# Optimization experiments

Hardware: AMD Instinct MI355X
Metric: run time of the kernel (lower is better)

The kernel has to match this reference:

```python
import jax, jax.numpy as jnp
import numpy as np

B, T, D, NH = 2, 2048, 2048, 16
HID = D  # hidden_dim must equal emb_dim for the source's fc2(x1) to type-check
HD = D // NH
EPS = 1e-5


def setup_inputs() -> dict:
    key = jax.random.key(0)
    ks = jax.random.split(key, 16)
    s = 0.02
    inp = {
        "x": jax.random.normal(ks[0], (B, T, D), jnp.float32),
        "Wq": jax.random.normal(ks[1], (D, D), jnp.float32) * s,
        "bq": jnp.zeros((D,), jnp.float32),
        "Wk": jax.random.normal(ks[2], (D, D), jnp.float32) * s,
        "bk": jnp.zeros((D,), jnp.float32),
        "Wv": jax.random.normal(ks[3], (D, D), jnp.float32) * s,
        "bv": jnp.zeros((D,), jnp.float32),
        "Wo": jax.random.normal(ks[4], (D, D), jnp.float32) * s,
        "bo": jnp.zeros((D,), jnp.float32),
        "scale1": jnp.ones((D,), jnp.float32),
        "scale2": jnp.ones((D,), jnp.float32),
        "W1": jax.random.normal(ks[5], (D, HID), jnp.float32) * s,
        "W2": jax.random.normal(ks[6], (D, HID), jnp.float32) * s,  # fc2: Linear(emb_dim, hidden_dim)
        "W3": jax.random.normal(ks[7], (HID, D), jnp.float32) * s,
    }
    return inp


def _rmsnorm(x, scale):
    m = jnp.mean(x * x, axis=-1, keepdims=True)
    return scale * (x * jax.lax.rsqrt(m + EPS))


def _attention(x, Wq, bq, Wk, bk, Wv, bv, Wo, bo):
    b, t, _ = x.shape
    q = (x @ Wq + bq).reshape(b, t, NH, HD)
    k = (x @ Wk + bk).reshape(b, t, NH, HD)
    v = (x @ Wv + bv).reshape(b, t, NH, HD)
    # energy: [B, H, T, T]; softmax over keys, scaled by 1/sqrt(head_dim); NO causal mask in source
    energy = jnp.einsum("bqhd,bkhd->bhqk", q, k) / jnp.sqrt(jnp.float32(HD))
    attn = jax.nn.softmax(energy, axis=-1)
    out = jnp.einsum("bhqk,bkhd->bqhd", attn, v).reshape(b, t, D)
    return out @ Wo + bo


def _ffn(x, W1, W2, W3):
    x1 = x @ W1                       # [B,T,HID]
    x2 = x1 @ W2                      # source quirk: fc2 applied to x1 (hidden_dim == emb_dim)
    return (x1 * jax.nn.sigmoid(x1) * x2) @ W3


def reference(x, Wq, bq, Wk, bk, Wv, bv, Wo, bo, scale1, scale2, W1, W2, W3):
    shortcut = x
    h = _rmsnorm(x, scale1)
    h = _attention(h, Wq, bq, Wk, bk, Wv, bv, Wo, bo)
    h = shortcut + h
    h = _rmsnorm(h, scale2)
    h = _ffn(h, W1, W2, W3)
    # source adds the ORIGINAL input again (shortcut never reassigned)
    return h + shortcut
```

## Files before the change

kernel.cpp:

```cpp
#include <hip/hip_runtime.h>

typedef __bf16 bf16x8 __attribute__((ext_vector_type(8)));
typedef __bf16 bf16x4v __attribute__((ext_vector_type(4)));
typedef float  f32x4  __attribute__((ext_vector_type(4)));

#define LDS_AS(p) ((__attribute__((address_space(3))) void*)(p))
#define GLB_AS(p) ((const __attribute__((address_space(1))) void*)(p))

struct TP { const float* s[7]; __bf16* d[7]; };
__global__ __launch_bounds__(256) void transpose_convert_all(TP p) {
  const float* __restrict__ W = p.s[blockIdx.z];
  __bf16* __restrict__ Wt = p.d[blockIdx.z];
  __shared__ float tile[32][33];
  const int tx = threadIdx.x & 31, ty = threadIdx.x >> 5;
  const int n0 = blockIdx.x * 32, k0 = blockIdx.y * 32;
#pragma unroll
  for (int j = 0; j < 4; ++j)
    tile[ty + j * 8][tx] = W[(size_t)(k0 + ty + j * 8) * 2048 + n0 + tx];
  __syncthreads();
#pragma unroll
  for (int j = 0; j < 4; ++j)
    Wt[(size_t)(n0 + ty + j * 8) * 2048 + k0 + tx] = (__bf16)tile[tx][ty + j * 8];
}

__global__ __launch_bounds__(256) void rmsnorm_k(
    const float* __restrict__ x, const float* __restrict__ scale,
    __bf16* __restrict__ out) {
  const int row = blockIdx.x, t = threadIdx.x;
  const float4* xr = (const float4*)(x + (size_t)row * 2048);
  float4 a = xr[t], b2 = xr[t + 256];
  float ss = a.x * a.x + a.y * a.y + a.z * a.z + a.w * a.w +
             b2.x * b2.x + b2.y * b2.y + b2.z * b2.z + b2.w * b2.w;
#pragma unroll
  for (int ofs = 32; ofs; ofs >>= 1) ss += __shfl_xor(ss, ofs, 64);
  __shared__ float red[4];
  if ((t & 63) == 0) red[t >> 6] = ss;
  __syncthreads();
  ss = red[0] + red[1] + red[2] + red[3];
  const float rs = rsqrtf(ss * (1.f / 2048.f) + 1e-5f);
  const float4* sr = (const float4*)scale;
  float4 s1 = sr[t], s2 = sr[t + 256];
  __bf16* orow = out + (size_t)row * 2048;
  orow[t * 4 + 0] = (__bf16)(a.x * rs * s1.x);
  orow[t * 4 + 1] = (__bf16)(a.y * rs * s1.y);
  orow[t * 4 + 2] = (__bf16)(a.z * rs * s1.z);
  orow[t * 4 + 3] = (__bf16)(a.w * rs * s1.w);
  orow[(t + 256) * 4 + 0] = (__bf16)(b2.x * rs * s2.x);
  orow[(t + 256) * 4 + 1] = (__bf16)(b2.y * rs * s2.y);
  orow[(t + 256) * 4 + 2] = (__bf16)(b2.z * rs * s2.z);
  orow[(t + 256) * 4 + 3] = (__bf16)(b2.w * rs * s2.w);
}

template <bool OUTF32, bool HASBIAS, bool HASRES, bool SILU>
__global__ __launch_bounds__(256) void gemm_bt(
    const __bf16* __restrict__ A, const __bf16* __restrict__ Bt,
    const float* __restrict__ bias, const float* __restrict__ res,
    const __bf16* __restrict__ ew, void* __restrict__ Cout,
    int M, int N, int Kd) {
  __shared__ __attribute__((aligned(16))) __bf16 As[2][128 * 32];
  __shared__ __attribute__((aligned(16))) __bf16 Bs[2][128 * 32];
  const int tid = threadIdx.x;
  const int w = tid >> 6, l = tid & 63;
  const int M0 = blockIdx.y * 128, N0 = blockIdx.x * 128;
  const int wr = w >> 1, wc = w & 1;
  const int lm = l & 15, lq = l >> 4;

  f32x4 acc[4][4];
#pragma unroll
  for (int mt = 0; mt < 4; ++mt)
#pragma unroll
    for (int nt = 0; nt < 4; ++nt)
#pragma unroll
      for (int e = 0; e < 4; ++e) acc[mt][nt][e] = 0.f;

  const int offA0 = (w * 2 + 0) * 1024 + l * 16;
  const int offA1 = (w * 2 + 1) * 1024 + l * 16;
  const int row0 = offA0 >> 6, kb0 = offA0 & 63;
  const int row1 = offA1 >> 6, kb1 = offA1 & 63;
  const int nIt = Kd >> 5;

  auto stage = [&](int k0, int bsel) {
    const char* ga0 = (const char*)(A + (size_t)(M0 + row0) * Kd + k0) + kb0;
    const char* ga1 = (const char*)(A + (size_t)(M0 + row1) * Kd + k0) + kb1;
    const char* gb0 = (const char*)(Bt + (size_t)(N0 + row0) * Kd + k0) + kb0;
    const char* gb1 = (const char*)(Bt + (size_t)(N0 + row1) * Kd + k0) + kb1;
    __builtin_amdgcn_global_load_lds(GLB_AS(ga0), LDS_AS(((char*)As[bsel]) + (w * 2 + 0) * 1024), 16, 0, 0);
    __builtin_amdgcn_global_load_lds(GLB_AS(ga1), LDS_AS(((char*)As[bsel]) + (w * 2 + 1) * 1024), 16, 0, 0);
    __builtin_amdgcn_global_load_lds(GLB_AS(gb0), LDS_AS(((char*)Bs[bsel]) + (w * 2 + 0) * 1024), 16, 0, 0);
    __builtin_amdgcn_global_load_lds(GLB_AS(gb1), LDS_AS(((char*)Bs[bsel]) + (w * 2 + 1) * 1024), 16, 0, 0);
  };

  stage(0, 0);
  for (int it = 0; it < nIt; ++it) {
    __syncthreads();
    if (it + 1 < nIt) stage((it + 1) * 32, (it + 1) & 1);
    const __bf16* Ab = As[it & 1];
    const __bf16* Bb = Bs[it & 1];
    bf16x8 af[4], bfr[4];
#pragma unroll
    for (int mt = 0; mt < 4; ++mt)
      af[mt] = *(const bf16x8*)(Ab + (wr * 64 + mt * 16 + lm) * 32 + lq * 8);
#pragma unroll
    for (int nt = 0; nt < 4; ++nt)
      bfr[nt] = *(const bf16x8*)(Bb + (wc * 64 + nt * 16 + lm) * 32 + lq * 8);
#pragma unroll
    for (int mt = 0; mt < 4; ++mt)
#pragma unroll
      for (int nt = 0; nt < 4; ++nt)
        acc[mt][nt] = __builtin_amdgcn_mfma_f32_16x16x32_bf16(af[mt], bfr[nt], acc[mt][nt], 0, 0, 0);
  }

  const int lr = lq * 4;
#pragma unroll
  for (int mt = 0; mt < 4; ++mt) {
#pragma unroll
    for (int nt = 0; nt < 4; ++nt) {
      const int col = N0 + wc * 64 + nt * 16 + lm;
      float bv = 0.f;
      if (HASBIAS) bv = bias[col];
#pragma unroll
      for (int i = 0; i < 4; ++i) {
        const int row = M0 + wr * 64 + mt * 16 + lr + i;
        const size_t off = (size_t)row * N + col;
        float v = acc[mt][nt][i] + bv;
        if (HASRES) v += res[off];
        if (SILU) {
          const float x1v = (float)ew[off];
          v = x1v * (1.f / (1.f + __expf(-x1v))) * v;
        }
        if (OUTF32) ((float*)Cout)[off] = v;
        else ((__bf16*)Cout)[off] = (__bf16)v;
      }
    }
  }
}

__global__ __launch_bounds__(256) void gemm_qkv(
    const __bf16* __restrict__ A, const __bf16* __restrict__ Bt,
    const float* __restrict__ bq, const float* __restrict__ bk,
    const float* __restrict__ bv,
    __bf16* __restrict__ Qout, __bf16* __restrict__ Kout,
    __bf16* __restrict__ Vtout, int Kd) {
  __shared__ __attribute__((aligned(16))) __bf16 As[2][128 * 32];
  __shared__ __attribute__((aligned(16))) __bf16 Bs[2][128 * 32];
  const int tid = threadIdx.x;
  const int w = tid >> 6, l = tid & 63;
  const int M0 = blockIdx.y * 128, N0 = blockIdx.x * 128;
  const int wr = w >> 1, wc = w & 1;
  const int lm = l & 15, lq = l >> 4;

  f32x4 acc[4][4];
#pragma unroll
  for (int mt = 0; mt < 4; ++mt)
#pragma unroll
    for (int nt = 0; nt < 4; ++nt)
#pragma unroll
      for (int e = 0; e < 4; ++e) acc[mt][nt][e] = 0.f;

  const int offA0 = (w * 2 + 0) * 1024 + l * 16;
  const int offA1 = (w * 2 + 1) * 1024 + l * 16;
  const int row0 = offA0 >> 6, kb0 = offA0 & 63;
  const int row1 = offA1 >> 6, kb1 = offA1 & 63;
  const int nIt = Kd >> 5;

  auto stage = [&](int k0, int bsel) {
    const char* ga0 = (const char*)(A + (size_t)(M0 + row0) * Kd + k0) + kb0;
    const char* ga1 = (const char*)(A + (size_t)(M0 + row1) * Kd + k0) + kb1;
    const char* gb0 = (const char*)(Bt + (size_t)(N0 + row0) * Kd + k0) + kb0;
    const char* gb1 = (const char*)(Bt + (size_t)(N0 + row1) * Kd + k0) + kb1;
    __builtin_amdgcn_global_load_lds(GLB_AS(ga0), LDS_AS(((char*)As[bsel]) + (w * 2 + 0) * 1024), 16, 0, 0);
    __builtin_amdgcn_global_load_lds(GLB_AS(ga1), LDS_AS(((char*)As[bsel]) + (w * 2 + 1) * 1024), 16, 0, 0);
    __builtin_amdgcn_global_load_lds(GLB_AS(gb0), LDS_AS(((char*)Bs[bsel]) + (w * 2 + 0) * 1024), 16, 0, 0);
    __builtin_amdgcn_global_load_lds(GLB_AS(gb1), LDS_AS(((char*)Bs[bsel]) + (w * 2 + 1) * 1024), 16, 0, 0);
  };

  stage(0, 0);
  for (int it = 0; it < nIt; ++it) {
    __syncthreads();
    if (it + 1 < nIt) stage((it + 1) * 32, (it + 1) & 1);
    const __bf16* Ab = As[it & 1];
    const __bf16* Bb = Bs[it & 1];
    bf16x8 af[4], bfr[4];
#pragma unroll
    for (int mt = 0; mt < 4; ++mt)
      af[mt] = *(const bf16x8*)(Ab + (wr * 64 + mt * 16 + lm) * 32 + lq * 8);
#pragma unroll
    for (int nt = 0; nt < 4; ++nt)
      bfr[nt] = *(const bf16x8*)(Bb + (wc * 64 + nt * 16 + lm) * 32 + lq * 8);
#pragma unroll
    for (int mt = 0; mt < 4; ++mt)
#pragma unroll
      for (int nt = 0; nt < 4; ++nt)
        acc[mt][nt] = __builtin_amdgcn_mfma_f32_16x16x32_bf16(af[mt], bfr[nt], acc[mt][nt], 0, 0, 0);
  }

  const int lr = lq * 4;
  const int seg = N0 >> 11;
  const int nbase = N0 & 2047;
  const float* bb = (seg == 0) ? bq : ((seg == 1) ? bk : bv);
  if (seg < 2) {
    __bf16* dst = (seg == 0) ? Qout : Kout;
#pragma unroll
    for (int mt = 0; mt < 4; ++mt) {
#pragma unroll
      for (int nt = 0; nt < 4; ++nt) {
        const int col = nbase + wc * 64 + nt * 16 + lm;
        const float bvv = bb[col];
#pragma unroll
        for (int i = 0; i < 4; ++i) {
          const int row = M0 + wr * 64 + mt * 16 + lr + i;
          dst[(size_t)row * 2048 + col] = (__bf16)(acc[mt][nt][i] + bvv);
        }
      }
    }
  } else {
#pragma unroll
    for (int mt = 0; mt < 4; ++mt) {
#pragma unroll
      for (int nt = 0; nt < 4; ++nt) {
        const int col = nbase + wc * 64 + nt * 16 + lm;
        const float bvv = bb[col];
        const int rw0 = M0 + wr * 64 + mt * 16 + lr;
        const int bidx = rw0 >> 11, tok = rw0 & 2047;
        bf16x4v pk;
#pragma unroll
        for (int i = 0; i < 4; ++i) pk[i] = (__bf16)(acc[mt][nt][i] + bvv);
        *(bf16x4v*)(Vtout + ((size_t)(bidx * 2048 + col)) * 2048 + tok) = pk;
      }
    }
  }
}

__global__ __launch_bounds__(256, 2) void attn_mfma(
    const __bf16* __restrict__ Q, const __bf16* __restrict__ K,
    const __bf16* __restrict__ Vt, __bf16* __restrict__ O) {
  __shared__ __attribute__((aligned(16))) char KsL[2][16 * 1024];
  __shared__ __attribute__((aligned(16))) char VsL[2][16 * 1024];

  const int t = threadIdx.x;
  const int w = t >> 6, l = t & 63;
  const int lm = l & 15, quad = l >> 4;
  const int h = blockIdx.y, b = blockIdx.z;
  const int q0 = blockIdx.x * 128;
  const size_t Ds = 2048;
  const size_t hoff = (size_t)h * 128;
  const size_t bbase = (size_t)b * 2048;
  const int sl16 = ((lm << 2) | quad) * 16;
  const float SCL = 0.08838834764831845f * 1.4426950408889634f;

  const int krow = l >> 2, kcol = (l & 3) * 8;
  const int vth = l & 3, vd = l >> 2;

  bf16x8 qf[2][4];
#pragma unroll
  for (int ntq = 0; ntq < 2; ++ntq)
#pragma unroll
    for (int ks = 0; ks < 4; ++ks)
      qf[ntq][ks] = *(const bf16x8*)(Q + (bbase + q0 + w * 32 + ntq * 16 + lm) * Ds + hoff + ks * 32 + quad * 8);

  f32x4 oacc[2][8];
#pragma unroll
  for (int ntq = 0; ntq < 2; ++ntq)
#pragma unroll
    for (int nv = 0; nv < 8; ++nv)
#pragma unroll
      for (int e = 0; e < 4; ++e) oacc[ntq][nv][e] = 0.f;
  float lpart[2] = {0.f, 0.f};

  bf16x8 vreg[4];

  auto loadV = [&](int kt) {
#pragma unroll
    for (int i = 0; i < 4; ++i) {
      const int chunk = w * 4 + i;
      const int nv = chunk >> 1, c = chunk & 1;
      vreg[i] = *(const bf16x8*)(Vt + (bbase + hoff + nv * 16 + vd) * Ds + kt + c * 32 + vth * 8);
    }
  };
  auto stageK = [&](int kt, char* Kb) {
#pragma unroll
    for (int i = 0; i < 4; ++i) {
      const __bf16* src = K + (bbase + kt + i * 16 + krow) * Ds + hoff + w * 32 + kcol;
      __builtin_amdgcn_global_load_lds(GLB_AS(src), LDS_AS(Kb + (i * 4 + w) * 1024), 16, 0, 0);
    }
  };
  auto writeV = [&](char* Vb) {
    const int s0off = ((vd << 2) | ((vth & 1) * 2)) * 16 + (vth >> 1) * 8;
#pragma unroll
    for (int i = 0; i < 4; ++i) {
      char* base = Vb + (w * 4 + i) * 1024;
      uint4 u = *(const uint4*)&vreg[i];
      *(uint2*)(base + s0off) = make_uint2(u.x, u.y);
      *(uint2*)(base + s0off + 16) = make_uint2(u.z, u.w);
    }
  };

  loadV(0);
  stageK(0, KsL[0]);
  writeV(VsL[0]);

  for (int it = 0; it < 32; ++it) {
    __syncthreads();
    const int cur = it & 1;
    const bool more = (it + 1) < 32;
    if (more) { loadV((it + 1) * 64); stageK((it + 1) * 64, KsL[(it + 1) & 1]); }

    const char* Kb = KsL[cur];
    const char* Vb = VsL[cur];

    f32x4 st[4][2];
#pragma unroll
    for (int mtk = 0; mtk < 4; ++mtk)
#pragma unroll
      for (int ntq = 0; ntq < 2; ++ntq)
#pragma unroll
        for (int e = 0; e < 4; ++e) st[mtk][ntq][e] = 0.f;
#pragma unroll
    for (int ks = 0; ks < 4; ++ks) {
#pragma unroll
      for (int mtk = 0; mtk < 4; ++mtk) {
        bf16x8 kf = *(const bf16x8*)(Kb + (mtk * 4 + ks) * 1024 + sl16);
        st[mtk][0] = __builtin_amdgcn_mfma_f32_16x16x32_bf16(kf, qf[0][ks], st[mtk][0], 0, 0, 0);
        st[mtk][1] = __builtin_amdgcn_mfma_f32_16x16x32_bf16(kf, qf[1][ks], st[mtk][1], 0, 0, 0);
      }
    }

#pragma unroll
    for (int c = 0; c < 2; ++c) {
      bf16x8 pf[2];
#pragma unroll
      for (int ntq = 0; ntq < 2; ++ntq) {
#pragma unroll
        for (int half = 0; half < 2; ++half) {
          const f32x4 sv = st[c * 2 + half][ntq];
#pragma unroll
          for (int r = 0; r < 4; ++r) {
            const float p = exp2f(sv[r] * SCL);
            const __bf16 pb = (__bf16)p;
            pf[ntq][half * 4 + r] = pb;
            lpart[ntq] += (float)pb;
          }
        }
      }
#pragma unroll
      for (int nv = 0; nv < 8; ++nv) {
        bf16x8 vf = *(const bf16x8*)(Vb + (nv * 2 + c) * 1024 + sl16);
        oacc[0][nv] = __builtin_amdgcn_mfma_f32_16x16x32_bf16(pf[0], vf, oacc[0][nv], 0, 0, 0);
        oacc[1][nv] = __builtin_amdgcn_mfma_f32_16x16x32_bf16(pf[1], vf, oacc[1][nv], 0, 0, 0);
      }
    }

    if (more) writeV(VsL[(it + 1) & 1]);
  }

  float linv[2];
#pragma unroll
  for (int ntq = 0; ntq < 2; ++ntq) {
    float v = lpart[ntq];
    v += __shfl_xor(v, 16, 64);
    v += __shfl_xor(v, 32, 64);
    linv[ntq] = 1.f / v;
  }
  float oinv[2][4];
#pragma unroll
  for (int ntq = 0; ntq < 2; ++ntq)
#pragma unroll
    for (int r = 0; r < 4; ++r)
      oinv[ntq][r] = __shfl(linv[ntq], quad * 4 + r, 64);

#pragma unroll
  for (int ntq = 0; ntq < 2; ++ntq)
#pragma unroll
    for (int nv = 0; nv < 8; ++nv)
#pragma unroll
      for (int r = 0; r < 4; ++r) {
        const int qrow = q0 + w * 32 + ntq * 16 + quad * 4 + r;
        O[(bbase + qrow) * Ds + hoff + nv * 16 + lm] = (__bf16)(oacc[ntq][nv][r] * oinv[ntq][r]);
      }
}

extern "C" void kernel_launch(void* const* d_in, const int* in_sizes, int n_in,
                              void* d_out, int out_size, void* d_ws, size_t ws_size,
                              hipStream_t stream) {
  const float* x      = (const float*)d_in[0];
  const float* Wq     = (const float*)d_in[1];
  const float* bq     = (const float*)d_in[2];
  const float* Wk     = (const float*)d_in[3];
  const float* bk     = (const float*)d_in[4];
  const float* Wv     = (const float*)d_in[5];
  const float* bv     = (const float*)d_in[6];
  const float* Wo     = (const float*)d_in[7];
  const float* bo     = (const float*)d_in[8];
  const float* scale1 = (const float*)d_in[9];
  const float* scale2 = (const float*)d_in[10];
  const float* W1     = (const float*)d_in[11];
  const float* W2     = (const float*)d_in[12];
  const float* W3     = (const float*)d_in[13];

  const int M = 4096, N = 2048, Kd = 2048;
  char* ws = (char*)d_ws;
  const size_t WT_B = (size_t)2048 * 2048 * 2;
  const size_t ACT_B = (size_t)4096 * 2048 * 2;
  __bf16* wt[7];
  size_t off = 0;
  for (int i = 0; i < 7; ++i) { wt[i] = (__bf16*)(ws + off); off += WT_B; }
  __bf16* hn1  = (__bf16*)(ws + off); off += ACT_B;
  __bf16* Qb   = (__bf16*)(ws + off); off += ACT_B;
  __bf16* Kb   = (__bf16*)(ws + off); off += ACT_B;
  __bf16* VtG  = (__bf16*)(ws + off); off += ACT_B;
  __bf16* attn = (__bf16*)(ws + off); off += ACT_B;
  __bf16* hn2  = (__bf16*)(ws + off); off += ACT_B;
  __bf16* x1b  = (__bf16*)(ws + off); off += ACT_B;
  __bf16* fmb  = (__bf16*)(ws + off); off += ACT_B;

  dim3 tb(256);
  {
    TP p;
    p.s[0] = Wq; p.s[1] = Wk; p.s[2] = Wv; p.s[3] = Wo; p.s[4] = W1; p.s[5] = W2; p.s[6] = W3;
    for (int i = 0; i < 7; ++i) p.d[i] = wt[i];
    transpose_convert_all<<<dim3(64, 64, 7), tb, 0, stream>>>(p);
  }

  rmsnorm_k<<<4096, tb, 0, stream>>>(x, scale1, hn1);

  gemm_qkv<<<dim3(6144 / 128, M / 128), tb, 0, stream>>>(
      hn1, wt[0], bq, bk, bv, Qb, Kb, VtG, Kd);

  dim3 ag(2048 / 128, 16, 2);
  attn_mfma<<<ag, tb, 0, stream>>>(Qb, Kb, VtG, attn);

  dim3 gg(N / 128, M / 128);
  gemm_bt<true, true, true, false><<<gg, tb, 0, stream>>>(attn, wt[3], bo, x, nullptr, d_out, M, N, Kd);

  rmsnorm_k<<<4096, tb, 0, stream>>>((const float*)d_out, scale2, hn2);

  gemm_bt<false, false, false, false><<<gg, tb, 0, stream>>>(hn2, wt[4], nullptr, nullptr, nullptr, x1b, M, N, Kd);
  gemm_bt<false, false, false, true><<<gg, tb, 0, stream>>>(x1b, wt[5], nullptr, nullptr, x1b, fmb, M, N, Kd);
  gemm_bt<true, false, true, false><<<gg, tb, 0, stream>>>(fmb, wt[6], nullptr, x, nullptr, d_out, M, N, Kd);
}
```

Measured before the change: 647.6 us.

## Rewrite QKV GEMM with 256x256 tiles, 8 waves, swizzled LDS and interleaved prefetch

The fused QKV projection GEMM now uses 256x256 output tiles computed by 512 threads (8 waves in a 2x4 layout), with a BK=64 K-step. LDS is XOR-swizzled to avoid bank conflicts. Global-to-LDS loads for the next tiles are split into quarter stages interleaved with four MFMA quadrants under explicit barriers, waitcnt and setprio scheduling. Block IDs are remapped for L2 locality. This aims to raise MFMA utilization and reduce memory stalls, at the cost of heavy register pressure (128 accumulator floats per lane) and a fragile hand-tuned schedule.

```diff
diff --git a/kernel.cpp b/kernel.cpp
--- a/kernel.cpp
+++ b/kernel.cpp
@@ -135,96 +135,171 @@
   }
 }
 
-__global__ __launch_bounds__(256) void gemm_qkv(
+__global__ __launch_bounds__(512, 2) void gemm_qkv(
     const __bf16* __restrict__ A, const __bf16* __restrict__ Bt,
     const float* __restrict__ bq, const float* __restrict__ bk,
     const float* __restrict__ bv,
     __bf16* __restrict__ Qout, __bf16* __restrict__ Kout,
     __bf16* __restrict__ Vtout, int Kd) {
-  __shared__ __attribute__((aligned(16))) __bf16 As[2][128 * 32];
-  __shared__ __attribute__((aligned(16))) __bf16 Bs[2][128 * 32];
+  __shared__ __attribute__((aligned(16))) char lds[2][4][16384];
+
   const int tid = threadIdx.x;
   const int w = tid >> 6, l = tid & 63;
-  const int M0 = blockIdx.y * 128, N0 = blockIdx.x * 128;
-  const int wr = w >> 1, wc = w & 1;
+  const int wr = w >> 2, wc = w & 3;
   const int lm = l & 15, lq = l >> 4;
 
-  f32x4 acc[4][4];
-#pragma unroll
-  for (int mt = 0; mt < 4; ++mt)
-#pragma unroll
-    for (int nt = 0; nt < 4; ++nt)
-#pragma unroll
-      for (int e = 0; e < 4; ++e) acc[mt][nt][e] = 0.f;
-
-  const int offA0 = (w * 2 + 0) * 1024 + l * 16;
-  const int offA1 = (w * 2 + 1) * 1024 + l * 16;
-  const int row0 = offA0 >> 6, kb0 = offA0 & 63;
-  const int row1 = offA1 >> 6, kb1 = offA1 & 63;
-  const int nIt = Kd >> 5;
-
-  auto stage = [&](int k0, int bsel) {
-    const char* ga0 = (const char*)(A + (size_t)(M0 + row0) * Kd + k0) + kb0;
-    const char* ga1 = (const char*)(A + (size_t)(M0 + row1) * Kd + k0) + kb1;
-    const char* gb0 = (const char*)(Bt + (size_t)(N0 + row0) * Kd + k0) + kb0;
-    const char* gb1 = (const char*)(Bt + (size_t)(N0 + row1) * Kd + k0) + kb1;
-    __builtin_amdgcn_global_load_lds(GLB_AS(ga0), LDS_AS(((char*)As[bsel]) + (w * 2 + 0) * 1024), 16, 0, 0);
-    __builtin_amdgcn_global_load_lds(GLB_AS(ga1), LDS_AS(((char*)As[bsel]) + (w * 2 + 1) * 1024), 16, 0, 0);
-    __builtin_amdgcn_global_load_lds(GLB_AS(gb0), LDS_AS(((char*)Bs[bsel]) + (w * 2 + 0) * 1024), 16, 0, 0);
-    __builtin_amdgcn_global_load_lds(GLB_AS(gb1), LDS_AS(((char*)Bs[bsel]) + (w * 2 + 1) * 1024), 16, 0, 0);
+  int bid = blockIdx.y * 24 + blockIdx.x;
+  bid = (bid & 7) * 48 + (bid >> 3);
+  const int bx = bid % 24, by = bid / 24;
+  const int N0 = bx * 256, M0 = by * 256;
+
+  const int srow = w * 8 + (l >> 3);
+  const int scol = ((l & 7) ^ (l >> 3)) * 8;
+  const __bf16* aS = A + (size_t)(M0 + srow) * Kd + scol;
+  const __bf16* bS = Bt + (size_t)(N0 + srow) * Kd + scol;
+
+  auto stageHT = [&](int t, int s) {
+    char* dst = lds[t & 1][s] + w * 1024;
+    const __bf16* src = (s >= 2) ? (aS + (size_t)(s - 2) * 128 * Kd + t * 64)
+                                 : (bS + (size_t)s * 128 * Kd + t * 64);
+    __builtin_amdgcn_global_load_lds(GLB_AS(src), LDS_AS(dst), 16, 0, 0);
+    __builtin_amdgcn_global_load_lds(GLB_AS(src + (size_t)64 * Kd), LDS_AS(dst + 8192), 16, 0, 0);
   };
 
-  stage(0, 0);
-  for (int it = 0; it < nIt; ++it) {
-    __syncthreads();
-    if (it + 1 < nIt) stage((it + 1) * 32, (it + 1) & 1);
-    const __bf16* Ab = As[it & 1];
-    const __bf16* Bb = Bs[it & 1];
-    bf16x8 af[4], bfr[4];
-#pragma unroll
-    for (int mt = 0; mt < 4; ++mt)
-      af[mt] = *(const bf16x8*)(Ab + (wr * 64 + mt * 16 + lm) * 32 + lq * 8);
-#pragma unroll
-    for (int nt = 0; nt < 4; ++nt)
-      bfr[nt] = *(const bf16x8*)(Bb + (wc * 64 + nt * 16 + lm) * 32 + lq * 8);
-#pragma unroll
-    for (int mt = 0; mt < 4; ++mt)
-#pragma unroll
-      for (int nt = 0; nt < 4; ++nt)
-        acc[mt][nt] = __builtin_amdgcn_mfma_f32_16x16x32_bf16(af[mt], bfr[nt], acc[mt][nt], 0, 0, 0);
-  }
-
-  const int lr = lq * 4;
+  f32x4 acc[8][4];
+#pragma unroll
+  for (int m = 0; m < 8; ++m)
+#pragma unroll
+    for (int n = 0; n < 4; ++n)
+#pragma unroll
+      for (int e = 0; e < 4; ++e) acc[m][n][e] = 0.f;
+
+  const int swzr = (lm & 7) << 4;
+  const int c0 = (lq * 16) ^ swzr;
+  const int c1 = ((64 + lq * 16)) ^ swzr;
+  const int arow = lm * 128;
+  const int brow = ((wc & 1) * 64 + lm) * 128;
+
+  stageHT(0, 0); stageHT(0, 1); stageHT(0, 2); stageHT(0, 3);
+  stageHT(1, 0); stageHT(1, 1); stageHT(1, 2);
+  asm volatile("s_waitcnt vmcnt(6)" ::: "memory");
+  __builtin_amdgcn_s_barrier();
+
+  const int NT = Kd >> 6;
+  bf16x8 af[4][2], bfr[4][2];
+
+#define MFMA_QUAD(MB, NB)                                                          \
+  do {                                                                             \
+    _Pragma("unroll") for (int m = 0; m < 4; ++m)                                  \
+      _Pragma("unroll") for (int n = 0; n < 2; ++n) {                              \
+        acc[(MB) + m][(NB) + n] = __builtin_amdgcn_mfma_f32_16x16x32_bf16(         \
+            af[m][0], bfr[(NB) + n][0], acc[(MB) + m][(NB) + n], 0, 0, 0);         \
+        acc[(MB) + m][(NB) + n] = __builtin_amdgcn_mfma_f32_16x16x32_bf16(         \
+            af[m][1], bfr[(NB) + n][1], acc[(MB) + m][(NB) + n], 0, 0, 0);         \
+      }                                                                            \
+  } while (0)
+
+  for (int t = 0; t < NT; ++t) {
+    const char* Ab = lds[t & 1][2 + wr];
+    const char* Bb = lds[t & 1][wc >> 1];
+
+#pragma unroll
+    for (int m = 0; m < 4; ++m) {
+      af[m][0] = *(const bf16x8*)(Ab + arow + m * 2048 + c0);
+      af[m][1] = *(const bf16x8*)(Ab + arow + m * 2048 + c1);
+    }
+#pragma unroll
+    for (int n = 0; n < 4; ++n) {
+      bfr[n][0] = *(const bf16x8*)(Bb + brow + n * 2048 + c0);
+      bfr[n][1] = *(const bf16x8*)(Bb + brow + n * 2048 + c1);
+    }
+    if (t + 1 < NT) stageHT(t + 1, 3);
+    asm volatile("" ::: "memory");
+    __builtin_amdgcn_s_barrier();
+    asm volatile("s_waitcnt lgkmcnt(0)" ::: "memory");
+    __builtin_amdgcn_sched_barrier(0);
+    __builtin_amdgcn_s_setprio(1);
+    MFMA_QUAD(0, 0);
+    __builtin_amdgcn_sched_barrier(0);
+    __builtin_amdgcn_s_setprio(0);
+    asm volatile("" ::: "memory");
+    __builtin_amdgcn_s_barrier();
+
+    if (t + 2 < NT) stageHT(t + 2, 0);
+    asm volatile("" ::: "memory");
+    __builtin_amdgcn_s_barrier();
+    __builtin_amdgcn_sched_barrier(0);
+    __builtin_amdgcn_s_setprio(1);
+    MFMA_QUAD(0, 2);
+    __builtin_amdgcn_sched_barrier(0);
+    __builtin_amdgcn_s_setprio(0);
+    asm volatile("" ::: "memory");
+    __builtin_amdgcn_s_barrier();
+
+#pragma unroll
+    for (int m = 0; m < 4; ++m) {
+      af[m][0] = *(const bf16x8*)(Ab + arow + (m + 4) * 2048 + c0);
+      af[m][1] = *(const bf16x8*)(Ab + arow + (m + 4) * 2048 + c1);
+    }
+    if (t + 2 < NT) stageHT(t + 2, 1);
+    asm volatile("" ::: "memory");
+    __builtin_amdgcn_s_barrier();
+    asm volatile("s_waitcnt lgkmcnt(0)" ::: "memory");
+    __builtin_amdgcn_sched_barrier(0);
+    __builtin_amdgcn_s_setprio(1);
+    MFMA_QUAD(4, 0);
+    __builtin_amdgcn_sched_barrier(0);
+    __builtin_amdgcn_s_setprio(0);
+    asm volatile("" ::: "memory");
+    __builtin_amdgcn_s_barrier();
+
+    if (t + 2 < NT) stageHT(t + 2, 2);
+    asm volatile("" ::: "memory");
+    __builtin_amdgcn_s_barrier();
+    __builtin_amdgcn_sched_barrier(0);
+    __builtin_amdgcn_s_setprio(1);
+    MFMA_QUAD(4, 2);
+    __builtin_amdgcn_sched_barrier(0);
+    __builtin_amdgcn_s_setprio(0);
+    if (t + 2 < NT) {
+      asm volatile("s_waitcnt vmcnt(6)" ::: "memory");
+    } else {
+      asm volatile("s_waitcnt vmcnt(0)" ::: "memory");
+    }
+    __builtin_amdgcn_s_barrier();
+  }
+#undef MFMA_QUAD
+
   const int seg = N0 >> 11;
   const int nbase = N0 & 2047;
   const float* bb = (seg == 0) ? bq : ((seg == 1) ? bk : bv);
   if (seg < 2) {
     __bf16* dst = (seg == 0) ? Qout : Kout;
 #pragma unroll
-    for (int mt = 0; mt < 4; ++mt) {
-#pragma unroll
-      for (int nt = 0; nt < 4; ++nt) {
-        const int col = nbase + wc * 64 + nt * 16 + lm;
+    for (int m = 0; m < 8; ++m) {
+#pragma unroll
+      for (int n = 0; n < 4; ++n) {
+        const int col = nbase + wc * 64 + n * 16 + lm;
         const float bvv = bb[col];
 #pragma unroll
         for (int i = 0; i < 4; ++i) {
-          const int row = M0 + wr * 64 + mt * 16 + lr + i;
-          dst[(size_t)row * 2048 + col] = (__bf16)(acc[mt][nt][i] + bvv);
+          const int row = M0 + wr * 128 + m * 16 + lq * 4 + i;
+          dst[(size_t)row * 2048 + col] = (__bf16)(acc[m][n][i] + bvv);
         }
       }
     }
   } else {
 #pragma unroll
-    for (int mt = 0; mt < 4; ++mt) {
-#pragma unroll
-      for (int nt = 0; nt < 4; ++nt) {
-        const int col = nbase + wc * 64 + nt * 16 + lm;
+    for (int m = 0; m < 8; ++m) {
+#pragma unroll
+      for (int n = 0; n < 4; ++n) {
+        const int col = nbase + wc * 64 + n * 16 + lm;
         const float bvv = bb[col];
-        const int rw0 = M0 + wr * 64 + mt * 16 + lr;
+        const int rw0 = M0 + wr * 128 + m * 16 + lq * 4;
         const int bidx = rw0 >> 11, tok = rw0 & 2047;
         bf16x4v pk;
 #pragma unroll
-        for (int i = 0; i < 4; ++i) pk[i] = (__bf16)(acc[mt][nt][i] + bvv);
+        for (int i = 0; i < 4; ++i) pk[i] = (__bf16)(acc[m][n][i] + bvv);
         *(bf16x4v*)(Vtout + ((size_t)(bidx * 2048 + col)) * 2048 + tok) = pk;
       }
     }
@@ -423,7 +498,7 @@
 
   rmsnorm_k<<<4096, tb, 0, stream>>>(x, scale1, hn1);
 
-  gemm_qkv<<<dim3(6144 / 128, M / 128), tb, 0, stream>>>(
+  gemm_qkv<<<dim3(6144 / 256, M / 256), dim3(512), 0, stream>>>(
       hn1, wt[0], bq, bk, bv, Qb, Kb, VtG, Kd);
 
   dim3 ag(2048 / 128, 16, 2);
```

Result: no change. 636.0 us (-1.8%).
